# Optimization experiments

Measured on AMD Instinct MI355X. Metric: run time of the kernel, lower is better.

Reference implementation:

```python
import jax, jax.numpy as jnp
import numpy as np
import math

D_MODEL = 1024
N_HEAD = 16
D_FF = 4096
B, T, S = 2, 2048, 2048
LN_EPS = 1e-5


def _linear(x, w, b):
    # torch nn.Linear: y = x @ W.T + b, W: [out, in]
    return jnp.einsum('bsd,od->bso', x, w) + b


def _layer_norm(x, g, b):
    mu = jnp.mean(x, axis=-1, keepdims=True)
    var = jnp.var(x, axis=-1, keepdims=True)
    return (x - mu) * jax.lax.rsqrt(var + LN_EPS) * g + b


def _mha(xq, xkv, wq, bq, wk, bk, wv, bv, wo, bo, mask):
    Bq, Tq, D = xq.shape
    Tk = xkv.shape[1]
    dk = D // N_HEAD
    q = _linear(xq, wq, bq).reshape(Bq, Tq, N_HEAD, dk).transpose(0, 2, 1, 3)
    k = _linear(xkv, wk, bk).reshape(Bq, Tk, N_HEAD, dk).transpose(0, 2, 1, 3)
    v = _linear(xkv, wv, bv).reshape(Bq, Tk, N_HEAD, dk).transpose(0, 2, 1, 3)
    scores = jnp.einsum('bhqd,bhkd->bhqk', q, k) / math.sqrt(dk)
    if mask is not None:
        scores = jnp.where(mask == 0, jnp.asarray(-1e9, scores.dtype), scores)
    attn = jax.nn.softmax(scores, axis=-1)  # dropout is eval-mode identity
    out = jnp.einsum('bhqk,bhkd->bhqd', attn, v)
    out = out.transpose(0, 2, 1, 3).reshape(Bq, Tq, D)
    return _linear(out, wo, bo)


def setup_inputs() -> dict:
    key = jax.random.key(0)
    ks = jax.random.split(key, 20)
    sd = 0.02

    def w(k, shape):
        return (jax.random.normal(k, shape, dtype=jnp.float32) * sd)

    inp = {
        'x': jax.random.normal(ks[0], (B, T, D_MODEL), dtype=jnp.float32),
        'enc_output': jax.random.normal(ks[1], (B, S, D_MODEL), dtype=jnp.float32),
        # causal (future) mask for self-attention
        'tgt_mask': jnp.tril(jnp.ones((T, T), dtype=jnp.int32))[None, None, :, :].repeat(B, axis=0),
        # no source padding -> all ones
        'src_tgt_mask': jnp.ones((B, 1, T, S), dtype=jnp.int32),
        'sa_wq': w(ks[2], (D_MODEL, D_MODEL)), 'sa_bq': jnp.zeros((D_MODEL,), jnp.float32),
        'sa_wk': w(ks[3], (D_MODEL, D_MODEL)), 'sa_bk': jnp.zeros((D_MODEL,), jnp.float32),
        'sa_wv': w(ks[4], (D_MODEL, D_MODEL)), 'sa_bv': jnp.zeros((D_MODEL,), jnp.float32),
        'sa_wo': w(ks[5], (D_MODEL, D_MODEL)), 'sa_bo': jnp.zeros((D_MODEL,), jnp.float32),
        'ca_wq': w(ks[6], (D_MODEL, D_MODEL)), 'ca_bq': jnp.zeros((D_MODEL,), jnp.float32),
        'ca_wk': w(ks[7], (D_MODEL, D_MODEL)), 'ca_bk': jnp.zeros((D_MODEL,), jnp.float32),
        'ca_wv': w(ks[8], (D_MODEL, D_MODEL)), 'ca_bv': jnp.zeros((D_MODEL,), jnp.float32),
        'ca_wo': w(ks[9], (D_MODEL, D_MODEL)), 'ca_bo': jnp.zeros((D_MODEL,), jnp.float32),
        'ffn_w1': w(ks[10], (D_FF, D_MODEL)), 'ffn_b1': jnp.zeros((D_FF,), jnp.float32),
        'ffn_w2': w(ks[11], (D_MODEL, D_FF)), 'ffn_b2': jnp.zeros((D_MODEL,), jnp.float32),
        'ln1_g': jnp.ones((D_MODEL,), jnp.float32), 'ln1_b': jnp.zeros((D_MODEL,), jnp.float32),
        'ln2_g': jnp.ones((D_MODEL,), jnp.float32), 'ln2_b': jnp.zeros((D_MODEL,), jnp.float32),
        'ln3_g': jnp.ones((D_MODEL,), jnp.float32), 'ln3_b': jnp.zeros((D_MODEL,), jnp.float32),
    }
    return inp


def reference(x, enc_output, tgt_mask, src_tgt_mask,
              sa_wq, sa_bq, sa_wk, sa_bk, sa_wv, sa_bv, sa_wo, sa_bo,
              ca_wq, ca_bq, ca_wk, ca_bk, ca_wv, ca_bv, ca_wo, ca_bo,
              ffn_w1, ffn_b1, ffn_w2, ffn_b2,
              ln1_g, ln1_b, ln2_g, ln2_b, ln3_g, ln3_b):
    # masked self-attention + residual + LN
    a1 = _mha(x, x, sa_wq, sa_bq, sa_wk, sa_bk, sa_wv, sa_bv, sa_wo, sa_bo, tgt_mask)
    x = _layer_norm(x + a1, ln1_g, ln1_b)
    # cross-attention + residual + LN
    a2 = _mha(x, enc_output, ca_wq, ca_bq, ca_wk, ca_bk, ca_wv, ca_bv, ca_wo, ca_bo, src_tgt_mask)
    x = _layer_norm(x + a2, ln2_g, ln2_b)
    # FFN + residual + LN
    h = jax.nn.relu(_linear(x, ffn_w1, ffn_b1))
    f = _linear(h, ffn_w2, ffn_b2)
    x = _layer_norm(x + f, ln3_g, ln3_b)
    return x
```

## Files before the change

### kernel.cpp

```cpp
#include <hip/hip_runtime.h>
#include <stdint.h>

typedef uint16_t u16;
typedef __attribute__((ext_vector_type(8))) short short8;
typedef __attribute__((ext_vector_type(4))) short short4v;
typedef __attribute__((ext_vector_type(4))) float f32x4;
typedef __attribute__((ext_vector_type(2))) unsigned int u32x2;

#define GLB_AS __attribute__((address_space(1)))
#define LDS_AS __attribute__((address_space(3)))

__device__ __forceinline__ void gload_lds16(const void* g, void* l) {
  __builtin_amdgcn_global_load_lds((GLB_AS void*)(g), (LDS_AS void*)(l), 16, 0, 0);
}

__device__ __forceinline__ float bf2f(u16 u) {
  union { uint32_t i; float f; } v; v.i = ((uint32_t)u) << 16; return v.f;
}
__device__ __forceinline__ u16 f2bf(float f) {
  uint32_t x = __builtin_bit_cast(uint32_t, f);
  return (u16)((x + 0x7fffu + ((x >> 16) & 1u)) >> 16);
}
__device__ __forceinline__ uint32_t cvtpk(float lo, float hi) {
  uint32_t r;
  asm("v_cvt_pk_bf16_f32 %0, %1, %2" : "=v"(r) : "v"(lo), "v"(hi));
  return r;
}

struct CastJobs {
  const float* s[12];
  u16* d[12];
  int n[12];
};
__global__ __launch_bounds__(256) void cast_many(CastJobs j)
{
  const int job = blockIdx.y;
  const int i = (blockIdx.x * 256 + threadIdx.x) * 4;
  if (i >= j.n[job]) return;
  const float4 v = *(const float4*)(j.s[job] + i);
  short4v r;
  r[0] = (short)f2bf(v.x); r[1] = (short)f2bf(v.y);
  r[2] = (short)f2bf(v.z); r[3] = (short)f2bf(v.w);
  *(short4v*)(j.d[job] + i) = r;
}

__global__ __launch_bounds__(256) void vtrans(
    const u16* __restrict__ V, int vs, u16* __restrict__ Vt)
{
  __shared__ u16 tl[64][72];
  const int tid = threadIdx.x;
  const int b = blockIdx.z, h = blockIdx.y, t0 = blockIdx.x * 64;
#pragma unroll
  for (int it = 0; it < 2; ++it) {
    const int r = (tid >> 3) + it*32, c = (tid & 7) * 8;
    short8 vv = *(const short8*)(V + (size_t)(b*2048 + t0 + r)*vs + h*64 + c);
    *(short8*)(&tl[r][c]) = vv;
  }
  __syncthreads();
#pragma unroll
  for (int it = 0; it < 2; ++it) {
    const int d = (tid >> 3) + it*32, t8 = (tid & 7) * 8;
    short8 ov;
#pragma unroll
    for (int j = 0; j < 8; ++j) ov[j] = (short)tl[t8 + j][d];
    *(short8*)(Vt + ((size_t)((b*16 + h)*64 + d))*2048 + t0 + t8) = ov;
  }
}

template<int RELU, int NSEG, int BN, int SCALEQ>
__global__ __launch_bounds__(256) void gemm_bt(
    const u16* __restrict__ A, const u16* __restrict__ W,
    const float* __restrict__ b0, const float* __restrict__ b1,
    const float* __restrict__ b2, u16* __restrict__ Y,
    int M, int N, int K)
{
  __shared__ __attribute__((aligned(16))) u16 lA[2][128*64];
  __shared__ __attribute__((aligned(16))) u16 lB[2][BN*64];
  const int tid  = threadIdx.x;
  const int lane = tid & 63, wv = tid >> 6;
  constexpr int WM = (BN == 128) ? 64 : 32;
  constexpr int MI = WM / 16;
  constexpr int BRND = BN / 32;
  const int wm = (BN == 128) ? (wv >> 1) : wv;
  const int wn = (BN == 128) ? (wv & 1) : 0;
  const int l16 = lane & 15, l4 = lane >> 4;
  const int rswz = (l16 & 7) << 4;

  const int gx = gridDim.x;
  int flat = blockIdx.y * gx + blockIdx.x;
  flat = (flat & 7) * ((gx * gridDim.y) >> 3) + (flat >> 3);
  const int bx = (flat % gx) * BN, by = (flat / gx) * 128;

  const f32x4 fzero = {0.f, 0.f, 0.f, 0.f};
  f32x4 acc[MI][4];
#pragma unroll
  for (int i = 0; i < MI; ++i)
#pragma unroll
    for (int j = 0; j < 4; ++j) acc[i][j] = fzero;

  const int o = wv*1024 + lane*16;

  auto stage = [&](int k0, int buf) {
#pragma unroll
    for (int r = 0; r < 4; ++r) {
      const int oo = r*4096 + o;
      const int row = oo >> 7;
      const int src = ((oo & 127) ^ ((row & 7) << 4)) >> 1;
      gload_lds16(A + (size_t)(by + row)*K + (k0 + src), (char*)lA[buf] + oo);
    }
#pragma unroll
    for (int r = 0; r < BRND; ++r) {
      const int oo = r*4096 + o;
      const int row = oo >> 7;
      const int src = ((oo & 127) ^ ((row & 7) << 4)) >> 1;
      gload_lds16(W + (size_t)(bx + row)*K + (k0 + src), (char*)lB[buf] + oo);
    }
  };

  stage(0, 0);
  const int KT = K >> 6;
  for (int kt = 0; kt < KT; ++kt) {
    const int cur = kt & 1;
    __syncthreads();
    short8 af[2][MI], bfv[2][4];
#pragma unroll
    for (int ks = 0; ks < 2; ++ks) {
      const int cb = (ks*64 + l4*16) ^ rswz;
#pragma unroll
      for (int i = 0; i < MI; ++i)
        af[ks][i]  = *(const short8*)((const char*)lA[cur] + (wm*WM + i*16 + l16)*128 + cb);
#pragma unroll
      for (int j = 0; j < 4; ++j)
        bfv[ks][j] = *(const short8*)((const char*)lB[cur] + (wn*64 + j*16 + l16)*128 + cb);
    }
    if (kt + 1 < KT) stage((kt + 1) << 6, cur ^ 1);
#pragma unroll
    for (int ks = 0; ks < 2; ++ks)
#pragma unroll
      for (int i = 0; i < MI; ++i)
#pragma unroll
        for (int j = 0; j < 4; ++j)
          acc[i][j] = __builtin_amdgcn_mfma_f32_16x16x32_bf16(af[ks][i], bfv[ks][j], acc[i][j], 0, 0, 0);
  }

  const float SCLF = 0.18033688f;
#pragma unroll
  for (int j = 0; j < 4; ++j) {
    const int col = bx + wn*64 + j*16 + l16;
    float bv;
    int seg = 0;
    if (NSEG == 1) bv = b0[col];
    else {
      seg = col >> 10;
      const int off = col & 1023;
      const float* bp = (seg == 0) ? b0 : ((seg == 1) ? b1 : b2);
      bv = bp[off];
    }
#pragma unroll
    for (int i = 0; i < MI; ++i) {
      const int r0 = by + wm*WM + i*16 + l4*4;
#pragma unroll
      for (int r = 0; r < 4; ++r) {
        float v = acc[i][j][r] + bv;
        if (RELU) v = v > 0.f ? v : 0.f;
        if (SCALEQ && (NSEG == 1 || seg == 0)) v *= SCLF;
        Y[(size_t)(r0 + r)*N + col] = f2bf(v);
      }
    }
  }
}

template<int CAUSAL, int QR>
__global__ __launch_bounds__(512, (QR == 16) ? 4 : 2) void attn_fwd(
    const u16* __restrict__ Q, int qs,
    const u16* __restrict__ K, int ks_,
    const u16* __restrict__ Vt, u16* __restrict__ O, int Tk)
{
  constexpr int NG = QR / 16;
  __shared__ __attribute__((aligned(16))) u16 lK[2][128*64];
  __shared__ __attribute__((aligned(16))) u16 lV[2][64*128];
  __shared__ __attribute__((aligned(16))) u16 lP[8][NG*1024];
  const int tid  = threadIdx.x;
  const int lane = tid & 63, wv = tid >> 6;
  const int l16 = lane & 15, l4 = lane >> 4;
  const int b = blockIdx.z, h = blockIdx.y;
  int strip;
  if (CAUSAL) {
    const int u = (blockIdx.x + blockIdx.z) & 15;
    strip = (u & 1) ? (15 - (u >> 1)) : (u >> 1);
  } else {
    strip = blockIdx.x;
  }
  const int Bq = strip * (8 * QR);
  const int qrow = Bq + wv*QR;

  short8 qf[NG][2];
#pragma unroll
  for (int g = 0; g < NG; ++g) {
    const u16* Qb = Q + (size_t)(b*2048 + qrow + g*16 + l16)*qs + h*64;
#pragma unroll
    for (int ks = 0; ks < 2; ++ks)
      qf[g][ks] = *(const short8*)(Qb + ks*32 + l4*8);
  }

  const f32x4 fzero = {0.f, 0.f, 0.f, 0.f};
  f32x4 accO[NG][4];
#pragma unroll
  for (int g = 0; g < NG; ++g)
#pragma unroll
    for (int i = 0; i < 4; ++i) accO[g][i] = fzero;
  float lrow[NG];
#pragma unroll
  for (int g = 0; g < NG; ++g) lrow[g] = 0.f;

  const int kend = CAUSAL ? (Bq + 8*QR) : Tk;
  const int nt = kend >> 7;
  const int qmax = qrow + QR - 1;
  const int srK = tid >> 3;
  const int scK = 8 * ((tid & 7) ^ (srK & 7));
  const int srV = tid >> 4;
  const int scV = 8 * ((tid & 15) ^ (srV & 7));
  const u16* KbG = K  + (size_t)(b*2048)*ks_ + h*64 + scK;
  const u16* VbG = Vt + ((size_t)((b*16 + h)*64 + srV))*2048 + scV;
  const int wvoff = (tid >> 6) * 1024;
  const int rswz = (l16 & 7) << 4;
  const int sbq = (lane & 48) + l4*4;

  char* const pbuf = (char*)lP + (tid >> 6) * (NG*2048);
  const int swzP = (l16 & 7) << 4;
  int wrA[4], rdA[2];
#pragma unroll
  for (int nf = 0; nf < 4; ++nf) wrA[nf] = l16*128 + ((nf*32 + l4*8) ^ swzP);
#pragma unroll
  for (int c = 0; c < 2; ++c)    rdA[c] = l16*128 + ((c*64 + l4*16) ^ swzP);

  auto readK = [&](int h2, int bb, short8 (&kf)[4][2]) {
#pragma unroll
    for (int nf = 0; nf < 4; ++nf) {
      const char* base = (const char*)lK[bb] + (h2*64 + nf*16 + l16)*128;
      kf[nf][0] = *(const short8*)(base + ((l4*16)      ^ rswz));
      kf[nf][1] = *(const short8*)(base + ((64 + l4*16) ^ rswz));
    }
  };

  auto compute64 = [&](int h2, int kvb, short8 (&kf)[4][2], int bb) {
#pragma unroll
    for (int g = 0; g < NG; ++g) {
      f32x4 sf[4];
      __builtin_amdgcn_s_setprio(1);
#pragma unroll
      for (int nf = 0; nf < 4; ++nf) {
        f32x4 s = fzero;
        s = __builtin_amdgcn_mfma_f32_16x16x32_bf16(kf[nf][0], qf[g][0], s, 0, 0, 0);
        s = __builtin_amdgcn_mfma_f32_16x16x32_bf16(kf[nf][1], qf[g][1], s, 0, 0, 0);
        sf[nf] = s;
      }
      __builtin_amdgcn_s_setprio(0);
      if (CAUSAL && (kvb + 63 > qrow + g*16)) {
        const int q = qrow + g*16 + l16;
#pragma unroll
        for (int nf = 0; nf < 4; ++nf)
#pragma unroll
          for (int r = 0; r < 4; ++r) {
            const int kv = kvb + nf*16 + l4*4 + r;
            if (kv > q) sf[nf][r] = -1e30f;
          }
      }
#pragma unroll
      for (int nf = 0; nf < 4; ++nf)
#pragma unroll
        for (int r = 0; r < 4; ++r)
          sf[nf][r] = exp2f(sf[nf][r]);
      float sm[4];
#pragma unroll
      for (int nf = 0; nf < 4; ++nf)
        sm[nf] = (sf[nf][0] + sf[nf][1]) + (sf[nf][2] + sf[nf][3]);
      lrow[g] += (sm[0] + sm[1]) + (sm[2] + sm[3]);
#pragma unroll
      for (int nf = 0; nf < 4; ++nf) {
        u32x2 w;
        w[0] = cvtpk(sf[nf][0], sf[nf][1]);
        w[1] = cvtpk(sf[nf][2], sf[nf][3]);
        *(u32x2*)(pbuf + g*2048 + wrA[nf]) = w;
      }
    }
#pragma unroll
    for (int c = 0; c < 2; ++c) {
      short8 pa[NG];
#pragma unroll
      for (int g = 0; g < NG; ++g)
        pa[g] = *(const short8*)(pbuf + g*2048 + rdA[c]);
      __builtin_amdgcn_s_setprio(1);
#pragma unroll
      for (int df = 0; df < 4; ++df) {
        const short8 vf = *(const short8*)((const char*)lV[bb] +
            (df*16 + l16)*256 + ((h2*128 + c*64 + l4*16) ^ rswz));
#pragma unroll
        for (int g = 0; g < NG; ++g)
          accO[g][df] = __builtin_amdgcn_mfma_f32_16x16x32_bf16(pa[g], vf, accO[g][df], 0, 0, 0);
      }
      __builtin_amdgcn_s_setprio(0);
    }
  };

#pragma unroll
  for (int r = 0; r < 2; ++r) {
    gload_lds16(KbG + (size_t)(r*64 + srK)*ks_, (char*)lK[0] + r*8192 + wvoff);
    gload_lds16(VbG + (size_t)(r*32)*2048,      (char*)lV[0] + r*8192 + wvoff);
  }

  for (int t = 0; t < nt; ++t) {
    const int bb = t & 1;
    const int kb = t << 7;
    __syncthreads();
    short8 kf[4][2];
    readK(0, bb, kf);
    if (t + 1 < nt) {
      const int kb2 = kb + 128;
#pragma unroll
      for (int r = 0; r < 2; ++r) {
        gload_lds16(KbG + (size_t)(kb2 + r*64 + srK)*ks_,
                    (char*)lK[bb^1] + r*8192 + wvoff);
        gload_lds16(VbG + (size_t)(r*32)*2048 + kb2,
                    (char*)lV[bb^1] + r*8192 + wvoff);
      }
    }
    compute64(0, kb, kf, bb);
    if (!CAUSAL || (kb + 64 <= qmax)) {
      readK(1, bb, kf);
      compute64(1, kb + 64, kf, bb);
    }
  }

#pragma unroll
  for (int g = 0; g < NG; ++g) {
    lrow[g] += __shfl_xor(lrow[g], 16);
    lrow[g] += __shfl_xor(lrow[g], 32);
    u16* Ob = O + (size_t)(b*2048 + qrow + g*16 + l4*4)*1024 + h*64;
#pragma unroll
    for (int r = 0; r < 4; ++r) {
      const float inv = 1.f / __shfl(lrow[g], sbq + r);
#pragma unroll
      for (int df = 0; df < 4; ++df)
        Ob[(size_t)r*1024 + df*16 + l16] = f2bf(accO[g][df][r] * inv);
    }
  }
}

template<int XF32, int OF32>
__global__ __launch_bounds__(256) void add_ln(
    const void* __restrict__ Xp, const u16* __restrict__ R,
    const float* __restrict__ G, const float* __restrict__ Bb,
    void* __restrict__ OUTp)
{
  const int row = blockIdx.x;
  const int tid = threadIdx.x;
  const size_t base = (size_t)row*1024 + tid*4;
  float xv[4];
  if (XF32) {
    const float4 t = *(const float4*)((const float*)Xp + base);
    xv[0] = t.x; xv[1] = t.y; xv[2] = t.z; xv[3] = t.w;
  } else {
    short4v t = *(const short4v*)((const u16*)Xp + base);
#pragma unroll
    for (int i = 0; i < 4; ++i) xv[i] = bf2f((u16)t[i]);
  }
  short4v rv = *(const short4v*)(R + base);
  float v[4], s = 0.f, s2 = 0.f;
#pragma unroll
  for (int i = 0; i < 4; ++i) {
    float t = xv[i] + bf2f((u16)rv[i]);
    v[i] = t; s += t; s2 += t*t;
  }
#pragma unroll
  for (int m = 1; m < 64; m <<= 1) { s += __shfl_xor(s, m); s2 += __shfl_xor(s2, m); }
  __shared__ float red[8];
  const int w = tid >> 6, lane = tid & 63;
  if (lane == 0) { red[w] = s; red[4 + w] = s2; }
  __syncthreads();
  s  = red[0] + red[1] + red[2] + red[3];
  s2 = red[4] + red[5] + red[6] + red[7];
  const float mu  = s * (1.f/1024.f);
  const float var = s2 * (1.f/1024.f) - mu*mu;
  const float rs  = rsqrtf(var + 1e-5f);
  if (OF32) {
    float4 ov;
    ov.x = (v[0]-mu)*rs*G[tid*4+0] + Bb[tid*4+0];
    ov.y = (v[1]-mu)*rs*G[tid*4+1] + Bb[tid*4+1];
    ov.z = (v[2]-mu)*rs*G[tid*4+2] + Bb[tid*4+2];
    ov.w = (v[3]-mu)*rs*G[tid*4+3] + Bb[tid*4+3];
    *(float4*)((float*)OUTp + base) = ov;
  } else {
    short4v ov;
#pragma unroll
    for (int i = 0; i < 4; ++i)
      ov[i] = (short)f2bf((v[i] - mu)*rs*G[tid*4+i] + Bb[tid*4+i]);
    *(short4v*)((u16*)OUTp + base) = ov;
  }
}

extern "C" void kernel_launch(void* const* d_in, const int* in_sizes, int n_in,
                              void* d_out, int out_size, void* d_ws, size_t ws_size,
                              hipStream_t stream)
{
  (void)in_sizes; (void)n_in; (void)out_size;
  const float* x    = (const float*)d_in[0];
  const float* enc  = (const float*)d_in[1];
  const float* sa_wq = (const float*)d_in[4];  const float* sa_bq = (const float*)d_in[5];
  const float* sa_wk = (const float*)d_in[6];  const float* sa_bk = (const float*)d_in[7];
  const float* sa_wv = (const float*)d_in[8];  const float* sa_bv = (const float*)d_in[9];
  const float* sa_wo = (const float*)d_in[10]; const float* sa_bo = (const float*)d_in[11];
  const float* ca_wq = (const float*)d_in[12]; const float* ca_bq = (const float*)d_in[13];
  const float* ca_wk = (const float*)d_in[14]; const float* ca_bk = (const float*)d_in[15];
  const float* ca_wv = (const float*)d_in[16]; const float* ca_bv = (const float*)d_in[17];
  const float* ca_wo = (const float*)d_in[18]; const float* ca_bo = (const float*)d_in[19];
  const float* w1 = (const float*)d_in[20];    const float* b1 = (const float*)d_in[21];
  const float* w2 = (const float*)d_in[22];    const float* b2 = (const float*)d_in[23];
  const float* ln1g = (const float*)d_in[24];  const float* ln1b = (const float*)d_in[25];
  const float* ln2g = (const float*)d_in[26];  const float* ln2b = (const float*)d_in[27];
  const float* ln3g = (const float*)d_in[28];  const float* ln3b = (const float*)d_in[29];
  float* out = (float*)d_out;

  char* ws = (char*)d_ws;
  const size_t MB = 1024*1024;
  u16* xb   = (u16*)(ws);
  u16* encb = (u16*)(ws + 8*MB);
  u16* wsab = (u16*)(ws + 16*MB);
  u16* wcab = (u16*)(ws + 24*MB);
  u16* x1   = (u16*)(ws + 32*MB);
  u16* ao   = (u16*)(ws + 40*MB);
  u16* tmp  = (u16*)(ws + 48*MB);
  u16* vt   = (u16*)(ws + 56*MB);
  u16* qkv  = (u16*)(ws + 64*MB);
  u16* kvb  = (u16*)(ws + 88*MB);
  u16* x2   = xb;
  u16* hb   = qkv;

  const bool bigws = ws_size >= (size_t)120*MB;
  u16* w1b = bigws ? (u16*)(ws + 104*MB) : encb;
  u16* w2b = bigws ? (u16*)(ws + 112*MB) : vt;

  const int NW = 1024*1024;
  const int NX = 4096*1024;
  dim3 blk(256);

  {
    CastJobs cj{};
    cj.s[0] = x;     cj.d[0] = xb;           cj.n[0] = NX;
    cj.s[1] = enc;   cj.d[1] = encb;         cj.n[1] = NX;
    cj.s[2] = sa_wq; cj.d[2] = wsab + 0*NW;  cj.n[2] = NW;
    cj.s[3] = sa_wk; cj.d[3] = wsab + 1*NW;  cj.n[3] = NW;
    cj.s[4] = sa_wv; cj.d[4] = wsab + 2*NW;  cj.n[4] = NW;
    cj.s[5] = sa_wo; cj.d[5] = wsab + 3*NW;  cj.n[5] = NW;
    cj.s[6] = ca_wq; cj.d[6] = wcab + 0*NW;  cj.n[6] = NW;
    cj.s[7] = ca_wk; cj.d[7] = wcab + 1*NW;  cj.n[7] = NW;
    cj.s[8] = ca_wv; cj.d[8] = wcab + 2*NW;  cj.n[8] = NW;
    cj.s[9] = ca_wo; cj.d[9] = wcab + 3*NW;  cj.n[9] = NW;
    int njobs = 10;
    if (bigws) {
      cj.s[10] = w1; cj.d[10] = w1b; cj.n[10] = NX;
      cj.s[11] = w2; cj.d[11] = w2b; cj.n[11] = NX;
      njobs = 12;
    }
    cast_many<<<dim3(NX/1024, njobs), blk, 0, stream>>>(cj);
  }

  const int M = 4096;
  dim3 gN64(16, 32);
  dim3 gQKV(24, 32);
  dim3 gKV(16, 32);
  dim3 gF1(32, 32);
  dim3 gAttn(16, 16, 2);
  dim3 gT(32, 16, 2);
  dim3 blk512(512);

  gemm_bt<0,3,128,1><<<gQKV, blk, 0, stream>>>(xb, wsab, sa_bq, sa_bk, sa_bv, qkv, M, 3072, 1024);
  vtrans<<<gT, blk, 0, stream>>>(qkv + 2048, 3072, vt);
  attn_fwd<1,16><<<gAttn, blk512, 0, stream>>>(qkv, 3072, qkv + 1024, 3072, vt, ao, 2048);
  gemm_bt<0,1,64,0><<<gN64, blk, 0, stream>>>(ao, wsab + 3*NW, sa_bo, sa_bo, sa_bo, tmp, M, 1024, 1024);
  add_ln<1,0><<<4096, blk, 0, stream>>>(x, tmp, ln1g, ln1b, x1);

  gemm_bt<0,1,64,1><<<gN64, blk, 0, stream>>>(x1, wcab + 0*NW, ca_bq, ca_bq, ca_bq, qkv, M, 1024, 1024);
  gemm_bt<0,2,128,0><<<gKV, blk, 0, stream>>>(encb, wcab + 1*NW, ca_bk, ca_bv, ca_bv, kvb, M, 2048, 1024);
  vtrans<<<gT, blk, 0, stream>>>(kvb + 1024, 2048, vt);
  attn_fwd<0,16><<<gAttn, blk512, 0, stream>>>(qkv, 1024, kvb, 2048, vt, ao, 2048);
  if (!bigws) {
    CastJobs cj{};
    cj.s[0] = w1; cj.d[0] = w1b; cj.n[0] = NX;
    cj.s[1] = w2; cj.d[1] = w2b; cj.n[1] = NX;
    cast_many<<<dim3(NX/1024, 2), blk, 0, stream>>>(cj);
  }
  gemm_bt<0,1,64,0><<<gN64, blk, 0, stream>>>(ao, wcab + 3*NW, ca_bo, ca_bo, ca_bo, tmp, M, 1024, 1024);
  add_ln<0,0><<<4096, blk, 0, stream>>>(x1, tmp, ln2g, ln2b, x2);

  gemm_bt<1,1,128,0><<<gF1, blk, 0, stream>>>(x2, w1b, b1, b1, b1, hb, M, 4096, 1024);
  gemm_bt<0,1,64,0><<<gN64, blk, 0, stream>>>(hb, w2b, b2, b2, b2, tmp, M, 1024, 4096);
  add_ln<0,1><<<4096, blk, 0, stream>>>(x2, tmp, ln3g, ln3b, out);
}
```

Before: 325.5 us.

## Fuse V transpose into projection GEMM epilogue and use one-wave-per-row LayerNorm

The QKV and cross-attention KV GEMM epilogues now write the V segment directly in transposed [b,h,d,t] layout, which removes both standalone vtrans kernels along with their extra read and write of V. The add+LayerNorm kernel is restructured so each wave handles one row with 16 elements per lane. That removes the LDS reduction and __syncthreads and uses wider vector loads and stores. The transposed epilogue writes 8-byte strided chunks, which may coalesce worse than the row-major stores.

```diff
diff --git a/kernel.cpp b/kernel.cpp
--- a/kernel.cpp
+++ b/kernel.cpp
@@ -44,34 +44,12 @@
   *(short4v*)(j.d[job] + i) = r;
 }
 
-__global__ __launch_bounds__(256) void vtrans(
-    const u16* __restrict__ V, int vs, u16* __restrict__ Vt)
-{
-  __shared__ u16 tl[64][72];
-  const int tid = threadIdx.x;
-  const int b = blockIdx.z, h = blockIdx.y, t0 = blockIdx.x * 64;
-#pragma unroll
-  for (int it = 0; it < 2; ++it) {
-    const int r = (tid >> 3) + it*32, c = (tid & 7) * 8;
-    short8 vv = *(const short8*)(V + (size_t)(b*2048 + t0 + r)*vs + h*64 + c);
-    *(short8*)(&tl[r][c]) = vv;
-  }
-  __syncthreads();
-#pragma unroll
-  for (int it = 0; it < 2; ++it) {
-    const int d = (tid >> 3) + it*32, t8 = (tid & 7) * 8;
-    short8 ov;
-#pragma unroll
-    for (int j = 0; j < 8; ++j) ov[j] = (short)tl[t8 + j][d];
-    *(short8*)(Vt + ((size_t)((b*16 + h)*64 + d))*2048 + t0 + t8) = ov;
-  }
-}
-
-template<int RELU, int NSEG, int BN, int SCALEQ>
+template<int RELU, int NSEG, int BN, int SCALEQ, int VT>
 __global__ __launch_bounds__(256) void gemm_bt(
     const u16* __restrict__ A, const u16* __restrict__ W,
     const float* __restrict__ b0, const float* __restrict__ b1,
     const float* __restrict__ b2, u16* __restrict__ Y,
+    u16* __restrict__ VTp,
     int M, int N, int K)
 {
   __shared__ __attribute__((aligned(16))) u16 lA[2][128*64];
@@ -159,12 +137,21 @@
 #pragma unroll
     for (int i = 0; i < MI; ++i) {
       const int r0 = by + wm*WM + i*16 + l4*4;
-#pragma unroll
-      for (int r = 0; r < 4; ++r) {
-        float v = acc[i][j][r] + bv;
-        if (RELU) v = v > 0.f ? v : 0.f;
-        if (SCALEQ && (NSEG == 1 || seg == 0)) v *= SCLF;
-        Y[(size_t)(r0 + r)*N + col] = f2bf(v);
+      if (VT > 0 && seg == VT) {
+        const int dcol = col - (VT << 10);
+        const int bb = r0 >> 11, t0 = r0 & 2047;
+        short4v pv;
+#pragma unroll
+        for (int r = 0; r < 4; ++r) pv[r] = (short)f2bf(acc[i][j][r] + bv);
+        *(short4v*)(VTp + ((size_t)((bb*16 + (dcol >> 6))*64 + (dcol & 63)))*2048 + t0) = pv;
+      } else {
+#pragma unroll
+        for (int r = 0; r < 4; ++r) {
+          float v = acc[i][j][r] + bv;
+          if (RELU) v = v > 0.f ? v : 0.f;
+          if (SCALEQ && (NSEG == 1 || seg == 0)) v *= SCLF;
+          Y[(size_t)(r0 + r)*N + col] = f2bf(v);
+        }
       }
     }
   }
@@ -353,49 +340,65 @@
     const float* __restrict__ G, const float* __restrict__ Bb,
     void* __restrict__ OUTp)
 {
-  const int row = blockIdx.x;
-  const int tid = threadIdx.x;
-  const size_t base = (size_t)row*1024 + tid*4;
-  float xv[4];
+  const int row  = blockIdx.x*4 + (threadIdx.x >> 6);
+  const int lane = threadIdx.x & 63;
+  const size_t base = (size_t)row*1024 + lane*16;
+  float v[16];
   if (XF32) {
-    const float4 t = *(const float4*)((const float*)Xp + base);
-    xv[0] = t.x; xv[1] = t.y; xv[2] = t.z; xv[3] = t.w;
+#pragma unroll
+    for (int k = 0; k < 4; ++k) {
+      const float4 t = *(const float4*)((const float*)Xp + base + k*4);
+      v[k*4+0] = t.x; v[k*4+1] = t.y; v[k*4+2] = t.z; v[k*4+3] = t.w;
+    }
   } else {
-    short4v t = *(const short4v*)((const u16*)Xp + base);
-#pragma unroll
-    for (int i = 0; i < 4; ++i) xv[i] = bf2f((u16)t[i]);
-  }
-  short4v rv = *(const short4v*)(R + base);
-  float v[4], s = 0.f, s2 = 0.f;
-#pragma unroll
-  for (int i = 0; i < 4; ++i) {
-    float t = xv[i] + bf2f((u16)rv[i]);
-    v[i] = t; s += t; s2 += t*t;
-  }
+#pragma unroll
+    for (int k = 0; k < 2; ++k) {
+      short8 t = *(const short8*)((const u16*)Xp + base + k*8);
+#pragma unroll
+      for (int i = 0; i < 8; ++i) v[k*8+i] = bf2f((u16)t[i]);
+    }
+  }
+#pragma unroll
+  for (int k = 0; k < 2; ++k) {
+    short8 t = *(const short8*)(R + base + k*8);
+#pragma unroll
+    for (int i = 0; i < 8; ++i) v[k*8+i] += bf2f((u16)t[i]);
+  }
+  float s = 0.f, s2 = 0.f;
+#pragma unroll
+  for (int i = 0; i < 16; ++i) { s += v[i]; s2 += v[i]*v[i]; }
 #pragma unroll
   for (int m = 1; m < 64; m <<= 1) { s += __shfl_xor(s, m); s2 += __shfl_xor(s2, m); }
-  __shared__ float red[8];
-  const int w = tid >> 6, lane = tid & 63;
-  if (lane == 0) { red[w] = s; red[4 + w] = s2; }
-  __syncthreads();
-  s  = red[0] + red[1] + red[2] + red[3];
-  s2 = red[4] + red[5] + red[6] + red[7];
   const float mu  = s * (1.f/1024.f);
   const float var = s2 * (1.f/1024.f) - mu*mu;
   const float rs  = rsqrtf(var + 1e-5f);
+  float gg[16], bb_[16];
+#pragma unroll
+  for (int k = 0; k < 4; ++k) {
+    const float4 g4 = *(const float4*)(G  + lane*16 + k*4);
+    const float4 b4 = *(const float4*)(Bb + lane*16 + k*4);
+    gg[k*4+0]=g4.x; gg[k*4+1]=g4.y; gg[k*4+2]=g4.z; gg[k*4+3]=g4.w;
+    bb_[k*4+0]=b4.x; bb_[k*4+1]=b4.y; bb_[k*4+2]=b4.z; bb_[k*4+3]=b4.w;
+  }
   if (OF32) {
-    float4 ov;
-    ov.x = (v[0]-mu)*rs*G[tid*4+0] + Bb[tid*4+0];
-    ov.y = (v[1]-mu)*rs*G[tid*4+1] + Bb[tid*4+1];
-    ov.z = (v[2]-mu)*rs*G[tid*4+2] + Bb[tid*4+2];
-    ov.w = (v[3]-mu)*rs*G[tid*4+3] + Bb[tid*4+3];
-    *(float4*)((float*)OUTp + base) = ov;
+#pragma unroll
+    for (int k = 0; k < 4; ++k) {
+      float4 ov;
+      ov.x = (v[k*4+0]-mu)*rs*gg[k*4+0] + bb_[k*4+0];
+      ov.y = (v[k*4+1]-mu)*rs*gg[k*4+1] + bb_[k*4+1];
+      ov.z = (v[k*4+2]-mu)*rs*gg[k*4+2] + bb_[k*4+2];
+      ov.w = (v[k*4+3]-mu)*rs*gg[k*4+3] + bb_[k*4+3];
+      *(float4*)((float*)OUTp + base + k*4) = ov;
+    }
   } else {
-    short4v ov;
-#pragma unroll
-    for (int i = 0; i < 4; ++i)
-      ov[i] = (short)f2bf((v[i] - mu)*rs*G[tid*4+i] + Bb[tid*4+i]);
-    *(short4v*)((u16*)OUTp + base) = ov;
+#pragma unroll
+    for (int k = 0; k < 2; ++k) {
+      short8 ov;
+#pragma unroll
+      for (int i = 0; i < 8; ++i)
+        ov[i] = (short)f2bf((v[k*8+i]-mu)*rs*gg[k*8+i] + bb_[k*8+i]);
+      *(short8*)((u16*)OUTp + base + k*8) = ov;
+    }
   }
 }
 
@@ -471,18 +474,15 @@
   dim3 gKV(16, 32);
   dim3 gF1(32, 32);
   dim3 gAttn(16, 16, 2);
-  dim3 gT(32, 16, 2);
   dim3 blk512(512);
 
-  gemm_bt<0,3,128,1><<<gQKV, blk, 0, stream>>>(xb, wsab, sa_bq, sa_bk, sa_bv, qkv, M, 3072, 1024);
-  vtrans<<<gT, blk, 0, stream>>>(qkv + 2048, 3072, vt);
+  gemm_bt<0,3,128,1,2><<<gQKV, blk, 0, stream>>>(xb, wsab, sa_bq, sa_bk, sa_bv, qkv, vt, M, 3072, 1024);
   attn_fwd<1,16><<<gAttn, blk512, 0, stream>>>(qkv, 3072, qkv + 1024, 3072, vt, ao, 2048);
-  gemm_bt<0,1,64,0><<<gN64, blk, 0, stream>>>(ao, wsab + 3*NW, sa_bo, sa_bo, sa_bo, tmp, M, 1024, 1024);
-  add_ln<1,0><<<4096, blk, 0, stream>>>(x, tmp, ln1g, ln1b, x1);
-
-  gemm_bt<0,1,64,1><<<gN64, blk, 0, stream>>>(x1, wcab + 0*NW, ca_bq, ca_bq, ca_bq, qkv, M, 1024, 1024);
-  gemm_bt<0,2,128,0><<<gKV, blk, 0, stream>>>(encb, wcab + 1*NW, ca_bk, ca_bv, ca_bv, kvb, M, 2048, 1024);
-  vtrans<<<gT, blk, 0, stream>>>(kvb + 1024, 2048, vt);
+  gemm_bt<0,1,64,0,0><<<gN64, blk, 0, stream>>>(ao, wsab + 3*NW, sa_bo, sa_bo, sa_bo, tmp, nullptr, M, 1024, 1024);
+  add_ln<1,0><<<1024, blk, 0, stream>>>(x, tmp, ln1g, ln1b, x1);
+
+  gemm_bt<0,1,64,1,0><<<gN64, blk, 0, stream>>>(x1, wcab + 0*NW, ca_bq, ca_bq, ca_bq, qkv, nullptr, M, 1024, 1024);
+  gemm_bt<0,2,128,0,1><<<gKV, blk, 0, stream>>>(encb, wcab + 1*NW, ca_bk, ca_bv, ca_bv, kvb, vt, M, 2048, 1024);
   attn_fwd<0,16><<<gAttn, blk512, 0, stream>>>(qkv, 1024, kvb, 2048, vt, ao, 2048);
   if (!bigws) {
     CastJobs cj{};
@@ -490,10 +490,10 @@
     cj.s[1] = w2; cj.d[1] = w2b; cj.n[1] = NX;
     cast_many<<<dim3(NX/1024, 2), blk, 0, stream>>>(cj);
   }
-  gemm_bt<0,1,64,0><<<gN64, blk, 0, stream>>>(ao, wcab + 3*NW, ca_bo, ca_bo, ca_bo, tmp, M, 1024, 1024);
-  add_ln<0,0><<<4096, blk, 0, stream>>>(x1, tmp, ln2g, ln2b, x2);
-
-  gemm_bt<1,1,128,0><<<gF1, blk, 0, stream>>>(x2, w1b, b1, b1, b1, hb, M, 4096, 1024);
-  gemm_bt<0,1,64,0><<<gN64, blk, 0, stream>>>(hb, w2b, b2, b2, b2, tmp, M, 1024, 4096);
-  add_ln<0,1><<<4096, blk, 0, stream>>>(x2, tmp, ln3g, ln3b, out);
-}
+  gemm_bt<0,1,64,0,0><<<gN64, blk, 0, stream>>>(ao, wcab + 3*NW, ca_bo, ca_bo, ca_bo, tmp, nullptr, M, 1024, 1024);
+  add_ln<0,0><<<1024, blk, 0, stream>>>(x1, tmp, ln2g, ln2b, x2);
+
+  gemm_bt<1,1,128,0,0><<<gF1, blk, 0, stream>>>(x2, w1b, b1, b1, b1, hb, nullptr, M, 4096, 1024);
+  gemm_bt<0,1,64,0,0><<<gN64, blk, 0, stream>>>(hb, w2b, b2, b2, b2, tmp, nullptr, M, 1024, 4096);
+  add_ln<0,1><<<1024, blk, 0, stream>>>(x2, tmp, ln3g, ln3b, out);
+}
```

Result: no change. 320.4 us (median of 2 runs) (-1.5%).
